# Kernel optimization log

Hardware: AMD Instinct MI355X
Metric: run time of the kernel (lower is better)

## Reference

```python
import jax, jax.numpy as jnp
import numpy as np

EPS = 1e-5  # BatchNorm eps (torch default)


def point_sample(feat, points):
    """Bilinear sample feat [B,C,Hf,Wf] at points [B,K,2] (x,y in [0,1]),
    matching F.grid_sample(2*p-1, mode='bilinear', padding_mode='zeros',
    align_corners=False)."""
    B, C, Hf, Wf = feat.shape
    x = points[..., 0] * Wf - 0.5  # [B,K] pixel coords
    y = points[..., 1] * Hf - 0.5
    x0f = jnp.floor(x); y0f = jnp.floor(y)
    wx = (x - x0f)[:, None, :]  # [B,1,K]
    wy = (y - y0f)[:, None, :]
    x0 = x0f.astype(jnp.int32); y0 = y0f.astype(jnp.int32)
    flat = feat.reshape(B, C, Hf * Wf)

    def gather(xi, yi):
        valid = ((xi >= 0) & (xi < Wf) & (yi >= 0) & (yi < Hf))[:, None, :]
        lin = jnp.clip(yi, 0, Hf - 1) * Wf + jnp.clip(xi, 0, Wf - 1)  # [B,K]
        idx = jnp.broadcast_to(lin[:, None, :], (B, C, lin.shape[1]))
        return jnp.take_along_axis(flat, idx, axis=2) * valid

    v00 = gather(x0, y0)
    v10 = gather(x0 + 1, y0)
    v01 = gather(x0, y0 + 1)
    v11 = gather(x0 + 1, y0 + 1)
    return (v00 * (1 - wx) * (1 - wy) + v10 * wx * (1 - wy)
            + v01 * (1 - wx) * wy + v11 * wx * wy)


def bn(x, g, b, m, v):
    # eval-mode BatchNorm1d over channel dim of [B,C,K]
    scale = (g / jnp.sqrt(v + EPS))[None, :, None]
    return (x - m[None, :, None]) * scale + b[None, :, None]


def setup_inputs() -> dict:
    key = jax.random.key(0)
    ks = jax.random.split(key, 20)
    B, H, W = 8, 512, 512
    Cf = 256
    d = {
        'uncertainty_map': jax.random.normal(ks[0], (B, 1, H, W), jnp.float32),
        'prev_mask': jax.random.uniform(ks[1], (B, 1, H, W), jnp.float32),
        'enc_f': jax.random.normal(ks[2], (B, Cf, 128, 128), jnp.float32),
        'w1': jax.random.normal(ks[3], (256, Cf + 1), jnp.float32) * 0.05,
        'b1': jax.random.normal(ks[4], (256,), jnp.float32) * 0.05,
        'g1': jnp.ones((256,), jnp.float32),
        'be1': jnp.zeros((256,), jnp.float32),
        'm1': jax.random.normal(ks[5], (256,), jnp.float32) * 0.1,
        'v1': jax.random.uniform(ks[6], (256,), jnp.float32) + 0.5,
        'w2': jax.random.normal(ks[7], (256, 256), jnp.float32) * 0.05,
        'b2': jax.random.normal(ks[8], (256,), jnp.float32) * 0.05,
        'g2': jnp.ones((256,), jnp.float32),
        'be2': jnp.zeros((256,), jnp.float32),
        'm2': jax.random.normal(ks[9], (256,), jnp.float32) * 0.1,
        'v2': jax.random.uniform(ks[10], (256,), jnp.float32) + 0.5,
        'w3': jax.random.normal(ks[11], (1, 256), jnp.float32) * 0.05,
        'b3': jax.random.normal(ks[12], (1,), jnp.float32) * 0.05,
    }
    return d


def reference(uncertainty_map, prev_mask, enc_f,
              w1, b1, g1, be1, m1, v1,
              w2, b2, g2, be2, m2, v2,
              w3, b3):
    B, C, H, W = prev_mask.shape
    K = H * W // 10
    # K least-uncertain points (topk largest=False)
    _, idx = jax.lax.top_k(-uncertainty_map.reshape(B, -1), K)  # [B,K] int32
    col = (idx % W).astype(jnp.float32)
    row = (idx // W).astype(jnp.float32)
    points = jnp.stack([(col + 0.5) / W, (row + 0.5) / H], axis=-1)  # [B,K,2]

    coarse = point_sample(prev_mask, points)  # [B,1,K]
    fine = point_sample(enc_f, points)        # [B,Cf,K]
    h = jnp.concatenate([coarse, fine], axis=1)  # [B,Cf+1,K]

    h = jax.nn.relu(bn(jnp.einsum('oc,bck->bok', w1, h) + b1[None, :, None], g1, be1, m1, v1))
    h = jax.nn.relu(bn(jnp.einsum('oc,bck->bok', w2, h) + b2[None, :, None], g2, be2, m2, v2))
    refined = jax.nn.sigmoid(jnp.einsum('oc,bck->bok', w3, h) + b3[None, :, None])  # [B,1,K]

    flat = prev_mask.reshape(B, C, H * W)
    bi = jnp.arange(B)[:, None, None]
    ci = jnp.arange(C)[None, :, None]
    out = flat.at[bi, ci, idx[:, None, :]].set(jnp.broadcast_to(refined, (B, C, K)))
    return out.reshape(B, C, H, W)
```

## Files before the change

kernel.cpp:

```cpp
#include <hip/hip_runtime.h>
#include <hip/hip_bf16.h>

#define HW_IMG 262144
#define KSEL   26214
#define NB     8
#define CF     256
#define LDACT  264
#define GBLK   410
#define MBLK   205
#define NPTS_PAD 26240

#define ACOL(c) ((c) ^ ((((c) >> 6) & 3) << 4))

typedef short    short8 __attribute__((ext_vector_type(8)));
typedef float    f32x4  __attribute__((ext_vector_type(4)));
typedef unsigned u32x2  __attribute__((ext_vector_type(2)));
typedef unsigned short u16x4 __attribute__((ext_vector_type(4)));

__device__ __forceinline__ unsigned f2key(float f){
    unsigned u = __builtin_bit_cast(unsigned, f);
    return (u & 0x80000000u) ? ~u : (u | 0x80000000u);
}
__device__ __forceinline__ unsigned short f2bf(float f){
    unsigned u = __builtin_bit_cast(unsigned, f);
    u = u + 0x7FFFu + ((u >> 16) & 1u);
    return (unsigned short)(u >> 16);
}
__device__ __forceinline__ float bf2f(unsigned short s){
    unsigned u = ((unsigned)s) << 16;
    return __builtin_bit_cast(float, u);
}

__global__ __launch_bounds__(256) void k_prep(
    const float* __restrict__ w1, const float* __restrict__ w2,
    const float* __restrict__ b1, const float* __restrict__ g1, const float* __restrict__ be1,
    const float* __restrict__ m1, const float* __restrict__ v1,
    const float* __restrict__ b2, const float* __restrict__ g2, const float* __restrict__ be2,
    const float* __restrict__ m2, const float* __restrict__ v2,
    unsigned short* __restrict__ w1p, unsigned short* __restrict__ w2p,
    float* __restrict__ c1, float* __restrict__ c2, float* __restrict__ w1c0)
{
    int tid = blockIdx.x * 256 + threadIdx.x;
    if (tid < 65536) {
        int o = tid >> 8, k = tid & 255;
        float scale = g1[o] * rsqrtf(v1[o] + 1e-5f);
        w1p[tid] = f2bf(w1[o * 257 + k + 1] * scale);
        if (k == 0) {
            c1[o] = (b1[o] - m1[o]) * scale + be1[o];
            w1c0[o] = w1[o * 257] * scale;
        }
    } else {
        int t2 = tid - 65536;
        int o = t2 >> 8;
        float scale = g2[o] * rsqrtf(v2[o] + 1e-5f);
        w2p[t2] = f2bf(w2[t2] * scale);
        if ((t2 & 255) == 0) c2[o] = (b2[o] - m2[o]) * scale + be2[o];
    }
}

__global__ __launch_bounds__(256, 3) void k_e1(
    const float* __restrict__ enc, const unsigned short* __restrict__ w1p,
    unsigned short* __restrict__ e1)
{
    __shared__ __align__(16) unsigned short actT[64][LDACT];
    __shared__ __align__(16) unsigned short tile[64][72];
    int wg = blockIdx.x;
    int b = wg & 7;
    int pixbase = (wg >> 3) * 64;
    int t = threadIdx.x;
    const float* src = enc + (size_t)b * CF * 16384;

    int pix = t & 63, cg = t >> 6;
#pragma unroll
    for (int cc = 0; cc < 4; cc++) {
#pragma unroll
        for (int i = 0; i < 16; i++) {
            int c = cc * 64 + cg * 16 + i;
            float v = __builtin_nontemporal_load(&src[(size_t)c * 16384 + pixbase + pix]);
            tile[pix][cg * 16 + i] = f2bf(v);
        }
        __syncthreads();
#pragma unroll
        for (int pass = 0; pass < 4; pass++) {
            int pl = pass * 16 + (t >> 4);
            int c4 = (t & 15) * 4;
            *(u16x4*)&actT[pl][ACOL(cc * 64 + c4)] = *(const u16x4*)&tile[pl][c4];
        }
        __syncthreads();
    }

    int w = t >> 6, l = t & 63;
    int lr = l & 15, lk = l >> 4;
    f32x4 acc[4][4];
#pragma unroll
    for (int m = 0; m < 4; m++)
#pragma unroll
        for (int n = 0; n < 4; n++) acc[m][n] = (f32x4){0.f, 0.f, 0.f, 0.f};
#pragma unroll
    for (int kk = 0; kk < 8; kk++) {
        int k0 = kk * 32 + lk * 8;
        int k0s = ACOL(k0);
        short8 afr[4], bfr[4];
#pragma unroll
        for (int m = 0; m < 4; m++)
            afr[m] = *(const short8*)(w1p + (size_t)(w * 64 + m * 16 + lr) * 256 + k0);
#pragma unroll
        for (int n = 0; n < 4; n++)
            bfr[n] = *(const short8*)&actT[n * 16 + lr][k0s];
#pragma unroll
        for (int m = 0; m < 4; m++)
#pragma unroll
            for (int n = 0; n < 4; n++)
                acc[m][n] = __builtin_amdgcn_mfma_f32_16x16x32_bf16(afr[m], bfr[n], acc[m][n], 0, 0, 0);
    }
    __syncthreads();

#pragma unroll
    for (int m = 0; m < 4; m++) {
        int chb = w * 64 + m * 16 + lk * 4;
        int chbs = ACOL(chb);
#pragma unroll
        for (int n = 0; n < 4; n++) {
            int p = n * 16 + lr;
            u32x2 pk;
            pk[0] = (unsigned)f2bf(acc[m][n][0]) | ((unsigned)f2bf(acc[m][n][1]) << 16);
            pk[1] = (unsigned)f2bf(acc[m][n][2]) | ((unsigned)f2bf(acc[m][n][3]) << 16);
            *(u32x2*)&actT[p][chbs] = pk;
        }
    }
    __syncthreads();

    unsigned short* dst = e1 + ((size_t)b * 16384 + pixbase) * CF;
#pragma unroll
    for (int i = 0; i < 8; i++) {
        int e = i * 2048 + t * 8;
        int pp = e >> 8, c = e & 255;
        short8 v = *(const short8*)&actT[pp][ACOL(c)];
        *(short8*)(dst + e) = v;
    }
}

__global__ __launch_bounds__(256) void k_histA(const float* __restrict__ unc, unsigned* __restrict__ hist)
{
    __shared__ unsigned lh[4][4096];
    int wg = blockIdx.x;
    int b = wg & 7, x = wg >> 3, t = threadIdx.x;
    int wv = t >> 6;
    for (int i = t; i < 4 * 4096; i += 256) ((unsigned*)lh)[i] = 0;
    __syncthreads();
    const float4* src = (const float4*)(unc + (size_t)b * HW_IMG + x * 4096);
    unsigned* mine = lh[wv];
#pragma unroll
    for (int j = 0; j < 4; j++) {
        float4 v = src[j * 256 + t];
        atomicAdd(&mine[f2key(v.x) >> 20], 1u);
        atomicAdd(&mine[f2key(v.y) >> 20], 1u);
        atomicAdd(&mine[f2key(v.z) >> 20], 1u);
        atomicAdd(&mine[f2key(v.w) >> 20], 1u);
    }
    __syncthreads();
    unsigned* gh = hist + (size_t)b * 4096;
    for (int i = t; i < 4096; i += 256) {
        unsigned c = lh[0][i] + lh[1][i] + lh[2][i] + lh[3][i];
        if (c) atomicAdd(&gh[i], c);
    }
}

__global__ __launch_bounds__(256) void k_histB(const float* __restrict__ unc,
    const unsigned* __restrict__ meta, unsigned* __restrict__ hist)
{
    __shared__ unsigned lh[4096];
    int wg = blockIdx.x;
    int b = wg & 7, x = wg >> 3, t = threadIdx.x;
    unsigned binA = meta[b * 8 + 0];
    for (int i = t; i < 4096; i += 256) lh[i] = 0;
    __syncthreads();
    const float4* src = (const float4*)(unc + (size_t)b * HW_IMG + x * 4096);
#pragma unroll
    for (int j = 0; j < 4; j++) {
        float4 v = src[j * 256 + t];
        unsigned k;
        k = f2key(v.x); if ((k >> 20) == binA) atomicAdd(&lh[(k >> 8) & 0xFFFu], 1u);
        k = f2key(v.y); if ((k >> 20) == binA) atomicAdd(&lh[(k >> 8) & 0xFFFu], 1u);
        k = f2key(v.z); if ((k >> 20) == binA) atomicAdd(&lh[(k >> 8) & 0xFFFu], 1u);
        k = f2key(v.w); if ((k >> 20) == binA) atomicAdd(&lh[(k >> 8) & 0xFFFu], 1u);
    }
    __syncthreads();
    unsigned* gh = hist + (size_t)b * 4096;
    for (int i = t; i < 4096; i += 256) { unsigned c = lh[i]; if (c) atomicAdd(&gh[i], c); }
}

__global__ __launch_bounds__(256) void k_histC(const float* __restrict__ unc,
    const unsigned* __restrict__ meta, unsigned* __restrict__ hist)
{
    __shared__ unsigned lh[256];
    int wg = blockIdx.x;
    int b = wg & 7, x = wg >> 3, t = threadIdx.x;
    unsigned pre24 = (meta[b * 8 + 0] << 12) | meta[b * 8 + 2];
    lh[t] = 0;
    __syncthreads();
    const float4* src = (const float4*)(unc + (size_t)b * HW_IMG + x * 4096);
#pragma unroll
    for (int j = 0; j < 4; j++) {
        float4 v = src[j * 256 + t];
        unsigned k;
        k = f2key(v.x); if ((k >> 8) == pre24) atomicAdd(&lh[k & 0xFFu], 1u);
        k = f2key(v.y); if ((k >> 8) == pre24) atomicAdd(&lh[k & 0xFFu], 1u);
        k = f2key(v.z); if ((k >> 8) == pre24) atomicAdd(&lh[k & 0xFFu], 1u);
        k = f2key(v.w); if ((k >> 8) == pre24) atomicAdd(&lh[k & 0xFFu], 1u);
    }
    __syncthreads();
    unsigned* gh = hist + (size_t)b * 4096;
    unsigned c = lh[t];
    if (c) atomicAdd(&gh[t], c);
}

__global__ __launch_bounds__(256) void k_find(const unsigned* __restrict__ hist,
    unsigned* __restrict__ meta, int per, int stage)
{
    int b = blockIdx.x, t = threadIdx.x;
    const unsigned* h = hist + (size_t)b * 4096;
    unsigned base = (stage == 0) ? 0u : meta[b * 8 + 2 * stage - 1];
    __shared__ unsigned seg[256], pref[256];
    unsigned s = 0;
    for (int i = 0; i < per; i++) s += h[t * per + i];
    seg[t] = s;
    __syncthreads();
    if (t == 0) { unsigned c = base; for (int i = 0; i < 256; i++) { pref[i] = c; c += seg[i]; } }
    __syncthreads();
    if (pref[t] < KSEL && KSEL <= pref[t] + seg[t]) {
        unsigned c = pref[t];
        for (int i = 0; i < per; i++) {
            unsigned cnt = h[t * per + i];
            if (c + cnt >= KSEL) {
                unsigned bin = (unsigned)(t * per + i);
                meta[b * 8 + 2 * stage] = bin;
                meta[b * 8 + 2 * stage + 1] = c;
                if (stage == 2)
                    meta[b * 8 + 6] = (meta[b * 8 + 0] << 20) | (meta[b * 8 + 2] << 8) | bin;
                break;
            }
            c += cnt;
        }
    }
}

__global__ __launch_bounds__(256) void k_count(const float* __restrict__ unc,
    const unsigned* __restrict__ meta, unsigned* __restrict__ cntL, unsigned* __restrict__ cntE)
{
    int wg = blockIdx.x;
    int b = wg & 7, blk = wg >> 3, t = threadIdx.x;
    unsigned pivot = meta[b * 8 + 6];
    const float4* src = (const float4*)(unc + (size_t)b * HW_IMG + blk * 1024);
    float4 v = src[t];
    unsigned k0 = f2key(v.x), k1 = f2key(v.y), k2 = f2key(v.z), k3 = f2key(v.w);
    unsigned cl = (k0 < pivot) + (k1 < pivot) + (k2 < pivot) + (k3 < pivot);
    unsigned ce = (k0 == pivot) + (k1 == pivot) + (k2 == pivot) + (k3 == pivot);
    __shared__ unsigned rl[256], re[256];
    rl[t] = cl; re[t] = ce; __syncthreads();
    for (int s = 128; s > 0; s >>= 1) { if (t < s) { rl[t] += rl[t + s]; re[t] += re[t + s]; } __syncthreads(); }
    if (t == 0) { cntL[b * 256 + blk] = rl[0]; cntE[b * 256 + blk] = re[0]; }
}

__global__ void k_scan(const unsigned* __restrict__ cntL, const unsigned* __restrict__ cntE,
                       unsigned* __restrict__ offL, unsigned* __restrict__ offE)
{
    int b = blockIdx.x;
    if (threadIdx.x == 0) {
        unsigned c = 0;
        for (int i = 0; i < 256; i++) { offL[b * 256 + i] = c; c += cntL[b * 256 + i]; }
        c = 0;
        for (int i = 0; i < 256; i++) { offE[b * 256 + i] = c; c += cntE[b * 256 + i]; }
    }
}

__global__ __launch_bounds__(256) void k_emit(const float* __restrict__ unc,
    const unsigned* __restrict__ meta, const unsigned* __restrict__ offL,
    const unsigned* __restrict__ offE, unsigned* __restrict__ sel)
{
    int wg = blockIdx.x;
    int b = wg & 7, blk = wg >> 3, t = threadIdx.x;
    unsigned pivot = meta[b * 8 + 6], cless = meta[b * 8 + 5], r = KSEL - cless;
    int base = blk * 1024 + t * 4;
    const float4* src = (const float4*)(unc + (size_t)b * HW_IMG + blk * 1024);
    float4 v = src[t];
    unsigned key[4] = { f2key(v.x), f2key(v.y), f2key(v.z), f2key(v.w) };
    unsigned cl = 0, ce = 0;
#pragma unroll
    for (int j = 0; j < 4; j++) { cl += (key[j] < pivot); ce += (key[j] == pivot); }
    __shared__ unsigned sL[256], sE[256];
    sL[t] = cl; sE[t] = ce; __syncthreads();
    for (int off = 1; off < 256; off <<= 1) {
        unsigned aL = (t >= off) ? sL[t - off] : 0u;
        unsigned aE = (t >= off) ? sE[t - off] : 0u;
        __syncthreads();
        sL[t] += aL; sE[t] += aE;
        __syncthreads();
    }
    unsigned posL = offL[b * 256 + blk] + sL[t] - cl;
    unsigned posE = offE[b * 256 + blk] + sE[t] - ce;
    unsigned* sb = sel + (size_t)b * KSEL;
#pragma unroll
    for (int j = 0; j < 4; j++) {
        if (key[j] < pivot) { sb[posL++] = (unsigned)(base + j); }
        else if (key[j] == pivot) { if (posE < r) sb[cless + posE] = (unsigned)(base + j); posE++; }
    }
}

__global__ __launch_bounds__(256) void k_gather(
    const unsigned* __restrict__ sel, const unsigned short* __restrict__ e1,
    const float* __restrict__ prev, const float* __restrict__ c1,
    const float* __restrict__ w1c0, unsigned short* __restrict__ gout)
{
    int wg = blockIdx.x;
    int b  = wg & 7;
    int pbase = (wg >> 3) * 64;
    int t = threadIdx.x;
    const unsigned* selb = sel + (size_t)b * KSEL;

    int wv2 = t >> 6, l2 = t & 63;
    int g = l2 >> 2, sub = l2 & 3;
    int p = wv2 * 16 + g;
    int gi = pbase + p; if (gi >= KSEL) gi = KSEL - 1;
    unsigned id = selb[gi];
    float cv = prev[(size_t)b * HW_IMG + id];
    int col = id & 511, row = (int)(id >> 9);
    float xf = (col - 1.5f) * 0.25f;
    float yf = (row - 1.5f) * 0.25f;
    float x0f = floorf(xf), y0f = floorf(yf);
    int x0 = (int)x0f, y0 = (int)y0f;
    float wx = xf - x0f, wy = yf - y0f;
    float wxa = (x0 >= 0) ? (1.f - wx) : 0.f;
    float wxb = (x0 <= 126) ? wx : 0.f;
    float wya = (y0 >= 0) ? (1.f - wy) : 0.f;
    float wyb = (y0 <= 126) ? wy : 0.f;
    int xc0 = x0 < 0 ? 0 : x0;
    int xc1 = (x0 + 1 > 127) ? 127 : x0 + 1;
    int yc0 = y0 < 0 ? 0 : y0;
    int yc1 = (y0 + 1 > 127) ? 127 : y0 + 1;
    float w00 = wxa * wya, w10 = wxb * wya, w01 = wxa * wyb, w11 = wxb * wyb;
    const unsigned short* bb = e1 + (size_t)b * 16384 * CF;
    const unsigned short* p00 = bb + (size_t)(yc0 * 128 + xc0) * CF + sub * 8;
    const unsigned short* p10 = bb + (size_t)(yc0 * 128 + xc1) * CF + sub * 8;
    const unsigned short* p01 = bb + (size_t)(yc1 * 128 + xc0) * CF + sub * 8;
    const unsigned short* p11 = bb + (size_t)(yc1 * 128 + xc1) * CF + sub * 8;
    unsigned short* dst = gout + ((size_t)b * NPTS_PAD + pbase + p) * CF + sub * 8;
#pragma unroll 4
    for (int ch = 0; ch < 8; ch++) {
        int off = ch * 32;
        int chb = sub * 8 + off;
        float4 ca = *(const float4*)(c1 + chb);
        float4 cb = *(const float4*)(c1 + chb + 4);
        float4 qa = *(const float4*)(w1c0 + chb);
        float4 qb = *(const float4*)(w1c0 + chb + 4);
        short8 va = *(const short8*)(p00 + off);
        short8 vb = *(const short8*)(p10 + off);
        short8 vc = *(const short8*)(p01 + off);
        short8 vd = *(const short8*)(p11 + off);
        short8 rr;
#pragma unroll
        for (int j = 0; j < 8; j++) {
            float f = w00 * bf2f((unsigned short)va[j]) + w10 * bf2f((unsigned short)vb[j])
                    + w01 * bf2f((unsigned short)vc[j]) + w11 * bf2f((unsigned short)vd[j]);
            float bias = (j < 4 ? ca[j] : cb[j - 4]) + (j < 4 ? qa[j] : qb[j - 4]) * cv;
            rr[j] = (short)f2bf(fmaxf(f + bias, 0.f));
        }
        __builtin_nontemporal_store(rr, (short8*)(dst + off));
    }
}

__global__ __launch_bounds__(512, 4) void k_mlp(
    const unsigned* __restrict__ sel, const unsigned short* __restrict__ gout,
    const unsigned short* __restrict__ w2p, const float* __restrict__ c2,
    const float* __restrict__ w3, const float* __restrict__ b3,
    float* __restrict__ out)
{
    __shared__ __align__(16) unsigned short act[128][LDACT];
    __shared__ float sPart[8][128];

    int wg = blockIdx.x;
    int b  = wg & 7;
    int pbase = (wg >> 3) * 128;
    int npts = KSEL - pbase; if (npts > 128) npts = 128;
    int t = threadIdx.x;
    const unsigned* selb = sel + (size_t)b * KSEL;

    const unsigned short* src = gout + ((size_t)b * NPTS_PAD + pbase) * CF;
#pragma unroll
    for (int i = 0; i < 8; i++) {
        int e = i * 4096 + t * 8;
        short8 v = __builtin_nontemporal_load((const short8*)(src + e));
        int pp = e >> 8, c = e & 255;
        *(short8*)&act[pp][ACOL(c)] = v;
    }
    __syncthreads();

    int w = t >> 6, l = t & 63;
    int lr = l & 15, lk = l >> 4;
    f32x4 acc[2][8];
#pragma unroll
    for (int m = 0; m < 2; m++)
#pragma unroll
        for (int n = 0; n < 8; n++) acc[m][n] = (f32x4){0.f, 0.f, 0.f, 0.f};

#pragma unroll
    for (int kk = 0; kk < 8; kk++) {
        int k0 = kk * 32 + lk * 8;
        int k0s = ACOL(k0);
        short8 afr[2], bfr[8];
#pragma unroll
        for (int m = 0; m < 2; m++)
            afr[m] = *(const short8*)(w2p + (size_t)(w * 32 + m * 16 + lr) * 256 + k0);
#pragma unroll
        for (int n = 0; n < 8; n++)
            bfr[n] = *(const short8*)&act[n * 16 + lr][k0s];
#pragma unroll
        for (int m = 0; m < 2; m++)
#pragma unroll
            for (int n = 0; n < 8; n++)
                acc[m][n] = __builtin_amdgcn_mfma_f32_16x16x32_bf16(afr[m], bfr[n], acc[m][n], 0, 0, 0);
    }

    float part[8] = {0.f, 0.f, 0.f, 0.f, 0.f, 0.f, 0.f, 0.f};
#pragma unroll
    for (int m = 0; m < 2; m++) {
        int chb = w * 32 + m * 16 + lk * 4;
#pragma unroll
        for (int r = 0; r < 4; r++) {
            float wr = w3[chb + r];
            float cr = c2[chb + r];
#pragma unroll
            for (int n = 0; n < 8; n++)
                part[n] += wr * fmaxf(acc[m][n][r] + cr, 0.f);
        }
    }
#pragma unroll
    for (int n = 0; n < 8; n++) {
        part[n] += __shfl_xor(part[n], 16);
        part[n] += __shfl_xor(part[n], 32);
    }
    if (lk == 0) {
#pragma unroll
        for (int n = 0; n < 8; n++) sPart[w][n * 16 + lr] = part[n];
    }
    __syncthreads();
    if (t < 128 && t < npts) {
        float tot = b3[0];
#pragma unroll
        for (int ww = 0; ww < 8; ww++) tot += sPart[ww][t];
        float refined = 1.f / (1.f + __expf(-tot));
        unsigned id = selb[pbase + t];
        __builtin_nontemporal_store(refined, &out[(size_t)b * HW_IMG + id]);
    }
}

extern "C" void kernel_launch(void* const* d_in, const int* in_sizes, int n_in,
                              void* d_out, int out_size, void* d_ws, size_t ws_size,
                              hipStream_t stream)
{
    (void)in_sizes; (void)n_in; (void)out_size; (void)ws_size;
    const float* unc  = (const float*)d_in[0];
    const float* prev = (const float*)d_in[1];
    const float* enc  = (const float*)d_in[2];
    const float* w1   = (const float*)d_in[3];
    const float* b1   = (const float*)d_in[4];
    const float* g1   = (const float*)d_in[5];
    const float* be1  = (const float*)d_in[6];
    const float* m1   = (const float*)d_in[7];
    const float* v1   = (const float*)d_in[8];
    const float* w2   = (const float*)d_in[9];
    const float* b2   = (const float*)d_in[10];
    const float* g2   = (const float*)d_in[11];
    const float* be2  = (const float*)d_in[12];
    const float* m2   = (const float*)d_in[13];
    const float* v2   = (const float*)d_in[14];
    const float* w3   = (const float*)d_in[15];
    const float* b3   = (const float*)d_in[16];
    float* out = (float*)d_out;

    char* ws = (char*)d_ws;
    size_t off = 0;
    auto alloc = [&](size_t bytes) { size_t o = off; off += (bytes + 255) & ~(size_t)255; return o; };
    size_t o_e1   = alloc((size_t)NB * 16384 * CF * 2);
    size_t o_gout = alloc((size_t)NB * NPTS_PAD * CF * 2);
    size_t o_w1p  = alloc((size_t)256 * 256 * 2);
    size_t o_w2p  = alloc((size_t)256 * 256 * 2);
    size_t o_c1   = alloc(256 * 4);
    size_t o_c2   = alloc(256 * 4);
    size_t o_w1c0 = alloc(256 * 4);
    size_t o_hist = alloc((size_t)3 * NB * 4096 * 4);
    size_t o_meta = alloc(NB * 8 * 4);
    size_t o_cntL = alloc(NB * 256 * 4);
    size_t o_cntE = alloc(NB * 256 * 4);
    size_t o_offL = alloc(NB * 256 * 4);
    size_t o_offE = alloc(NB * 256 * 4);
    size_t o_sel  = alloc((size_t)NB * KSEL * 4);

    unsigned short* e1p  = (unsigned short*)(ws + o_e1);
    unsigned short* goutp= (unsigned short*)(ws + o_gout);
    unsigned short* w1p  = (unsigned short*)(ws + o_w1p);
    unsigned short* w2p  = (unsigned short*)(ws + o_w2p);
    float* c1p = (float*)(ws + o_c1);
    float* c2p = (float*)(ws + o_c2);
    float* w1c0p = (float*)(ws + o_w1c0);
    unsigned* histA = (unsigned*)(ws + o_hist);
    unsigned* histB = histA + (size_t)NB * 4096;
    unsigned* histC = histB + (size_t)NB * 4096;
    unsigned* meta  = (unsigned*)(ws + o_meta);
    unsigned* cntL  = (unsigned*)(ws + o_cntL);
    unsigned* cntE  = (unsigned*)(ws + o_cntE);
    unsigned* offL  = (unsigned*)(ws + o_offL);
    unsigned* offE  = (unsigned*)(ws + o_offE);
    unsigned* sel   = (unsigned*)(ws + o_sel);

    hipMemsetAsync(ws + o_hist, 0, (size_t)3 * NB * 4096 * 4, stream);
    hipMemcpyAsync(d_out, (const void*)prev, (size_t)NB * HW_IMG * 4, hipMemcpyDeviceToDevice, stream);

    k_prep<<<512, 256, 0, stream>>>(w1, w2, b1, g1, be1, m1, v1, b2, g2, be2, m2, v2,
                                    w1p, w2p, c1p, c2p, w1c0p);
    k_e1  <<<2048, 256, 0, stream>>>(enc, w1p, e1p);

    k_histA<<<512, 256, 0, stream>>>(unc, histA);
    k_find <<<NB, 256, 0, stream>>>(histA, meta, 16, 0);
    k_histB<<<512, 256, 0, stream>>>(unc, meta, histB);
    k_find <<<NB, 256, 0, stream>>>(histB, meta, 16, 1);
    k_histC<<<512, 256, 0, stream>>>(unc, meta, histC);
    k_find <<<NB, 256, 0, stream>>>(histC, meta, 1, 2);
    k_count<<<2048, 256, 0, stream>>>(unc, meta, cntL, cntE);
    k_scan <<<NB, 64, 0, stream>>>(cntL, cntE, offL, offE);
    k_emit <<<2048, 256, 0, stream>>>(unc, meta, offL, offE, sel);

    k_gather<<<GBLK * NB, 256, 0, stream>>>(sel, e1p, prev, c1p, w1c0p, goutp);
    k_mlp   <<<MBLK * NB, 512, 0, stream>>>(sel, goutp, w2p, c2p, w3, b3, out);
}
```

Baseline: 226.4 us.

## Replace count/scan/emit selection with atomic-offset emit plus tie-fix pass

Merges the separate count, serial scan and emit kernels into one emit kernel that reserves output ranges per block with global atomics. Ties at the pivot go to a side buffer, and a small fix kernel ranks them by index so the lowest-index ties fill the remaining slots. The selected index order becomes nondeterministic, and the fix kernel's quadratic ranking can get slow when there are many ties. The histA kernel also drops from four per-wave shared histograms to two, and the gather kernel's nontemporal store becomes a plain store.

```diff
diff --git a/kernel.cpp b/kernel.cpp
--- a/kernel.cpp
+++ b/kernel.cpp
@@ -142,14 +142,14 @@
 
 __global__ __launch_bounds__(256) void k_histA(const float* __restrict__ unc, unsigned* __restrict__ hist)
 {
-    __shared__ unsigned lh[4][4096];
+    __shared__ unsigned lh[2][4096];
     int wg = blockIdx.x;
     int b = wg & 7, x = wg >> 3, t = threadIdx.x;
-    int wv = t >> 6;
-    for (int i = t; i < 4 * 4096; i += 256) ((unsigned*)lh)[i] = 0;
+    int half = t >> 7;
+    for (int i = t; i < 2 * 4096; i += 256) ((unsigned*)lh)[i] = 0;
     __syncthreads();
     const float4* src = (const float4*)(unc + (size_t)b * HW_IMG + x * 4096);
-    unsigned* mine = lh[wv];
+    unsigned* mine = lh[half];
 #pragma unroll
     for (int j = 0; j < 4; j++) {
         float4 v = src[j * 256 + t];
@@ -161,7 +161,7 @@
     __syncthreads();
     unsigned* gh = hist + (size_t)b * 4096;
     for (int i = t; i < 4096; i += 256) {
-        unsigned c = lh[0][i] + lh[1][i] + lh[2][i] + lh[3][i];
+        unsigned c = lh[0][i] + lh[1][i];
         if (c) atomicAdd(&gh[i], c);
     }
 }
@@ -245,42 +245,13 @@
     }
 }
 
-__global__ __launch_bounds__(256) void k_count(const float* __restrict__ unc,
-    const unsigned* __restrict__ meta, unsigned* __restrict__ cntL, unsigned* __restrict__ cntE)
+__global__ __launch_bounds__(256) void k_emit(const float* __restrict__ unc,
+    const unsigned* __restrict__ meta, unsigned* __restrict__ sel,
+    unsigned* __restrict__ eq, unsigned* __restrict__ ctr)
 {
     int wg = blockIdx.x;
     int b = wg & 7, blk = wg >> 3, t = threadIdx.x;
     unsigned pivot = meta[b * 8 + 6];
-    const float4* src = (const float4*)(unc + (size_t)b * HW_IMG + blk * 1024);
-    float4 v = src[t];
-    unsigned k0 = f2key(v.x), k1 = f2key(v.y), k2 = f2key(v.z), k3 = f2key(v.w);
-    unsigned cl = (k0 < pivot) + (k1 < pivot) + (k2 < pivot) + (k3 < pivot);
-    unsigned ce = (k0 == pivot) + (k1 == pivot) + (k2 == pivot) + (k3 == pivot);
-    __shared__ unsigned rl[256], re[256];
-    rl[t] = cl; re[t] = ce; __syncthreads();
-    for (int s = 128; s > 0; s >>= 1) { if (t < s) { rl[t] += rl[t + s]; re[t] += re[t + s]; } __syncthreads(); }
-    if (t == 0) { cntL[b * 256 + blk] = rl[0]; cntE[b * 256 + blk] = re[0]; }
-}
-
-__global__ void k_scan(const unsigned* __restrict__ cntL, const unsigned* __restrict__ cntE,
-                       unsigned* __restrict__ offL, unsigned* __restrict__ offE)
-{
-    int b = blockIdx.x;
-    if (threadIdx.x == 0) {
-        unsigned c = 0;
-        for (int i = 0; i < 256; i++) { offL[b * 256 + i] = c; c += cntL[b * 256 + i]; }
-        c = 0;
-        for (int i = 0; i < 256; i++) { offE[b * 256 + i] = c; c += cntE[b * 256 + i]; }
-    }
-}
-
-__global__ __launch_bounds__(256) void k_emit(const float* __restrict__ unc,
-    const unsigned* __restrict__ meta, const unsigned* __restrict__ offL,
-    const unsigned* __restrict__ offE, unsigned* __restrict__ sel)
-{
-    int wg = blockIdx.x;
-    int b = wg & 7, blk = wg >> 3, t = threadIdx.x;
-    unsigned pivot = meta[b * 8 + 6], cless = meta[b * 8 + 5], r = KSEL - cless;
     int base = blk * 1024 + t * 4;
     const float4* src = (const float4*)(unc + (size_t)b * HW_IMG + blk * 1024);
     float4 v = src[t];
@@ -289,6 +260,7 @@
 #pragma unroll
     for (int j = 0; j < 4; j++) { cl += (key[j] < pivot); ce += (key[j] == pivot); }
     __shared__ unsigned sL[256], sE[256];
+    __shared__ unsigned baseL, baseE;
     sL[t] = cl; sE[t] = ce; __syncthreads();
     for (int off = 1; off < 256; off <<= 1) {
         unsigned aL = (t >= off) ? sL[t - off] : 0u;
@@ -297,13 +269,36 @@
         sL[t] += aL; sE[t] += aE;
         __syncthreads();
     }
-    unsigned posL = offL[b * 256 + blk] + sL[t] - cl;
-    unsigned posE = offE[b * 256 + blk] + sE[t] - ce;
+    if (t == 255) {
+        baseL = atomicAdd(&ctr[b * 2 + 0], sL[255]);
+        baseE = atomicAdd(&ctr[b * 2 + 1], sE[255]);
+    }
+    __syncthreads();
+    unsigned posL = baseL + sL[t] - cl;
+    unsigned posE = baseE + sE[t] - ce;
     unsigned* sb = sel + (size_t)b * KSEL;
+    unsigned* eb = eq + (size_t)b * HW_IMG;
 #pragma unroll
     for (int j = 0; j < 4; j++) {
         if (key[j] < pivot) { sb[posL++] = (unsigned)(base + j); }
-        else if (key[j] == pivot) { if (posE < r) sb[cless + posE] = (unsigned)(base + j); posE++; }
+        else if (key[j] == pivot) { eb[posE++] = (unsigned)(base + j); }
+    }
+}
+
+__global__ __launch_bounds__(256) void k_fix(const unsigned* __restrict__ ctr,
+    const unsigned* __restrict__ eq, unsigned* __restrict__ sel)
+{
+    int b = blockIdx.x, t = threadIdx.x;
+    unsigned cless = ctr[b * 2 + 0];
+    unsigned n = ctr[b * 2 + 1];
+    unsigned r = KSEL - cless;
+    const unsigned* eb = eq + (size_t)b * HW_IMG;
+    unsigned* sb = sel + (size_t)b * KSEL;
+    for (unsigned i = t; i < n; i += 256) {
+        unsigned v = eb[i];
+        unsigned rank = 0;
+        for (unsigned j = 0; j < n; j++) rank += (eb[j] < v);
+        if (rank < r) sb[cless + rank] = v;
     }
 }
 
@@ -365,7 +360,7 @@
             float bias = (j < 4 ? ca[j] : cb[j - 4]) + (j < 4 ? qa[j] : qb[j - 4]) * cv;
             rr[j] = (short)f2bf(fmaxf(f + bias, 0.f));
         }
-        __builtin_nontemporal_store(rr, (short8*)(dst + off));
+        *(short8*)(dst + off) = rr;
     }
 }
 
@@ -488,12 +483,10 @@
     size_t o_c1   = alloc(256 * 4);
     size_t o_c2   = alloc(256 * 4);
     size_t o_w1c0 = alloc(256 * 4);
-    size_t o_hist = alloc((size_t)3 * NB * 4096 * 4);
+    size_t histBytes = (size_t)3 * NB * 4096 * 4 + NB * 2 * 4;
+    size_t o_hist = alloc(histBytes);
     size_t o_meta = alloc(NB * 8 * 4);
-    size_t o_cntL = alloc(NB * 256 * 4);
-    size_t o_cntE = alloc(NB * 256 * 4);
-    size_t o_offL = alloc(NB * 256 * 4);
-    size_t o_offE = alloc(NB * 256 * 4);
+    size_t o_eq   = alloc((size_t)NB * HW_IMG * 4);
     size_t o_sel  = alloc((size_t)NB * KSEL * 4);
 
     unsigned short* e1p  = (unsigned short*)(ws + o_e1);
@@ -506,14 +499,12 @@
     unsigned* histA = (unsigned*)(ws + o_hist);
     unsigned* histB = histA + (size_t)NB * 4096;
     unsigned* histC = histB + (size_t)NB * 4096;
+    unsigned* ctr   = histC + (size_t)NB * 4096;
     unsigned* meta  = (unsigned*)(ws + o_meta);
-    unsigned* cntL  = (unsigned*)(ws + o_cntL);
-    unsigned* cntE  = (unsigned*)(ws + o_cntE);
-    unsigned* offL  = (unsigned*)(ws + o_offL);
-    unsigned* offE  = (unsigned*)(ws + o_offE);
+    unsigned* eq    = (unsigned*)(ws + o_eq);
     unsigned* sel   = (unsigned*)(ws + o_sel);
 
-    hipMemsetAsync(ws + o_hist, 0, (size_t)3 * NB * 4096 * 4, stream);
+    hipMemsetAsync(ws + o_hist, 0, histBytes, stream);
     hipMemcpyAsync(d_out, (const void*)prev, (size_t)NB * HW_IMG * 4, hipMemcpyDeviceToDevice, stream);
 
     k_prep<<<512, 256, 0, stream>>>(w1, w2, b1, g1, be1, m1, v1, b2, g2, be2, m2, v2,
@@ -526,9 +517,8 @@
     k_find <<<NB, 256, 0, stream>>>(histB, meta, 16, 1);
     k_histC<<<512, 256, 0, stream>>>(unc, meta, histC);
     k_find <<<NB, 256, 0, stream>>>(histC, meta, 1, 2);
-    k_count<<<2048, 256, 0, stream>>>(unc, meta, cntL, cntE);
-    k_scan <<<NB, 64, 0, stream>>>(cntL, cntE, offL, offE);
-    k_emit <<<2048, 256, 0, stream>>>(unc, meta, offL, offE, sel);
+    k_emit <<<2048, 256, 0, stream>>>(unc, meta, sel, eq, ctr);
+    k_fix  <<<NB, 256, 0, stream>>>(ctr, eq, sel);
 
     k_gather<<<GBLK * NB, 256, 0, stream>>>(sel, e1p, prev, c1p, w1c0p, goutp);
     k_mlp   <<<MBLK * NB, 512, 0, stream>>>(sel, goutp, w2p, c2p, w3, b3, out);
```

Result: slower. 256.1 us (+13.1%).
